# Optimization experiments

Measured on AMD Instinct MI355X. Metric: run time of the kernel, lower is better.

Reference implementation:

```python
import jax, jax.numpy as jnp
import numpy as np

NTYPE = 4
NWAVE = 8
NORBIT = 128
NIPSIN = 3
CUTOFF = 5.0
NEIGH = 64
NB = 32
NATOM = 256
NPAIR_PER = NATOM * NEIGH  # pairs per molecule

# index_para: [0, 1,1,1, 2,...x9] -> length 1 + 3 + 9 = 13
INDEX_PARA = np.concatenate([np.zeros(1, np.int32)] + [np.full(3 ** i, i, np.int32) for i in range(1, NIPSIN)])
NPARA = INDEX_PARA.shape[0]  # 13


def setup_inputs() -> dict:
    key = jax.random.key(0)
    ks = jax.random.split(key, 12)
    cart = jax.random.normal(ks[0], (NB, NATOM, 3), dtype=jnp.float32)
    numatoms = jnp.full((NB,), NATOM, dtype=jnp.int32)
    species = jax.random.randint(ks[1], (NB * NATOM,), 0, NTYPE, dtype=jnp.int32)
    atom_index = jax.random.randint(ks[2], (2, NB, NPAIR_PER), 0, NATOM, dtype=jnp.int32)
    # small nonzero shifts so no pair has exactly zero distance
    shifts = 0.1 * jax.random.normal(ks[3], (NB, NPAIR_PER, 3), dtype=jnp.float32)
    rs = jax.random.uniform(ks[4], (NTYPE, NWAVE), dtype=jnp.float32) * CUTOFF
    inta = -jnp.abs(jax.random.normal(ks[5], (NTYPE, NWAVE), dtype=jnp.float32))
    params = jnp.ones((NTYPE, NWAVE), dtype=jnp.float32) / float(NEIGH)
    hyper = 0.1 * jax.random.normal(ks[6], (NIPSIN, NWAVE, NORBIT), dtype=jnp.float32)
    oc_w0 = 0.05 * jax.random.normal(ks[7], (NORBIT, NWAVE), dtype=jnp.float32)
    oc_e0 = 0.05 * jax.random.normal(ks[8], (NTYPE, NWAVE), dtype=jnp.float32)
    oc_w1 = 0.05 * jax.random.normal(ks[9], (NORBIT, NWAVE), dtype=jnp.float32)
    oc_e1 = 0.05 * jax.random.normal(ks[10], (NTYPE, NWAVE), dtype=jnp.float32)
    return {"cart": cart, "shifts": shifts, "rs": rs, "inta": inta, "params": params,
            "hyper": hyper, "oc_w0": oc_w0, "oc_e0": oc_e0, "oc_w1": oc_w1, "oc_e1": oc_e1,
            "numatoms": numatoms, "species": species, "atom_index": atom_index}


def _angular(dist_vec, f_cut):
    # dist_vec: (N, 3), f_cut: (N,) -> (NPARA, N)
    dv = dist_vec.T  # (3, N)
    ang = f_cut[None, :]  # (1, N)
    parts = [ang]
    for _ in range(1, NIPSIN):
        ang = (ang[:, None, :] * dv[None, :, :]).reshape(-1, ang.shape[-1])
        parts.append(ang)
    return jnp.concatenate(parts, axis=0)  # (13, N)


def reference(cart, shifts, rs, inta, params, hyper, oc_w0, oc_e0, oc_w1, oc_e1,
              numatoms, species, atom_index):
    nbatch, numatom, _ = cart.shape
    totnatom = nbatch * numatom
    # global pair indices: per-molecule neighbor indices + molecule offset
    offsets = jnp.arange(nbatch, dtype=atom_index.dtype) * numatom  # (nbatch,)
    idx12 = (atom_index + offsets[None, :, None]).reshape(2, -1)  # (2, Npair)
    cart_ = cart.reshape(-1, 3)  # (totnatom, 3)
    dist_vec = cart_[idx12[0]] - cart_[idx12[1]] + shifts.reshape(-1, 3)  # (Npair, 3)
    distances = jnp.linalg.norm(dist_vec, axis=-1)  # (Npair,)
    f_cut = jnp.square(0.5 * jnp.cos(distances * (jnp.pi / CUTOFF)) + 0.5)
    sp_pair = species[idx12[1]]  # (Npair,)
    # radial gaussian: exp(inta * (d - rs)^2), per-pair type gather
    radial = jnp.exp(inta[sp_pair] * jnp.square(distances[:, None] - rs[sp_pair]))  # (Npair, nwave)
    ang = _angular(dist_vec, f_cut)  # (NPARA, Npair)
    # orbital[i, j, k] = ang[j, i] * radial[i, k]
    orbital = ang.T[:, :, None] * radial[:, None, :]  # (Npair, NPARA, nwave)
    hyper_exp = hyper[jnp.asarray(INDEX_PARA)]  # (NPARA, nwave, norbit)

    def obtain(orb_coeff):
        worbital = orbital * orb_coeff[idx12[1]][:, None, :]  # gather + scale
        sum_worbital = jax.ops.segment_sum(worbital, idx12[0], num_segments=totnatom)
        hyper_worbital = jnp.einsum('ijk,jkm->ijm', sum_worbital, hyper_exp)
        return jnp.sum(jnp.square(hyper_worbital), axis=1)  # (totnatom, norbit)

    orb_coeff = params[species]  # (totnatom, nwave)
    density = obtain(orb_coeff)
    for w, e in ((oc_w0, oc_e0), (oc_w1, oc_e1)):
        orb_coeff = orb_coeff + jnp.tanh(density @ w + e[species])
        density = obtain(orb_coeff)
    return density
```

## Files before the change

### kernel.cpp

```cpp
#include <hip/hip_runtime.h>
#include <hip/hip_bf16.h>
#include <math.h>

#define NTYPE   4
#define NWAVE   8
#define NORBIT  128
#define NEIGH   64
#define NB      32
#define NATOM   256
#define NPP     (NATOM * NEIGH)
#define NPAIR   (NB * NPP)
#define TOTATOM (NB * NATOM)
#define NPARA   13

#define CHUNK   2048
#define BPB     8
#define NBLK    (NB * BPB)

__device__ __forceinline__ float fast_tanh(float x) {
    float ax = fabsf(x);
    float e  = __expf(-2.0f * ax);
    float r  = (1.0f - e) / (1.0f + e);
    return copysignf(r, x);
}

__global__ __launch_bounds__(256) void k_hist(const int* __restrict__ atom_index,
                                              int* __restrict__ histpart) {
    const int bl = blockIdx.x, t = threadIdx.x;
    const int b = bl >> 3, c = bl & 7;
    __shared__ int hist[NATOM];
    hist[t] = 0;
    __syncthreads();
    const int base = b * NPP + c * CHUNK;
#pragma unroll
    for (int k = 0; k < CHUNK / 256; k++) {
        int i = atom_index[base + t + k * 256];
        atomicAdd(&hist[i], 1);
    }
    __syncthreads();
    histpart[bl * NATOM + t] = hist[t];
}

__global__ __launch_bounds__(256) void k_offsets(const int* __restrict__ histpart,
                                                 int* __restrict__ startpart,
                                                 int* __restrict__ offs,
                                                 const int* __restrict__ species,
                                                 const float* __restrict__ params,
                                                 float* __restrict__ coeff0) {
    const int b = blockIdx.x, t = threadIdx.x;
    int h[BPB];
    int tot = 0;
#pragma unroll
    for (int c = 0; c < BPB; c++) {
        h[c] = histpart[(b * BPB + c) * NATOM + t];
        tot += h[c];
    }
    __shared__ int scan[NATOM];
    scan[t] = tot;
    __syncthreads();
    for (int d = 1; d < NATOM; d <<= 1) {
        int v = (t >= d) ? scan[t - d] : 0;
        __syncthreads();
        scan[t] += v;
        __syncthreads();
    }
    int run = b * NPP + (scan[t] - tot);
    offs[b * NATOM + t] = run;
    if (b == 0 && t == 0) offs[TOTATOM] = NPAIR;
#pragma unroll
    for (int c = 0; c < BPB; c++) {
        startpart[(b * BPB + c) * NATOM + t] = run;
        run += h[c];
    }
    int a = b * NATOM + t;
    int sp = species[a];
#pragma unroll
    for (int w = 0; w < NWAVE; w++) coeff0[a * NWAVE + w] = params[sp * NWAVE + w];
}

__global__ __launch_bounds__(256) void k_scatter(const int* __restrict__ atom_index,
                                                 const float* __restrict__ cart,
                                                 const float* __restrict__ shifts,
                                                 const int* __restrict__ species,
                                                 const int* __restrict__ startpart,
                                                 float4* __restrict__ rec) {
    const int bl = blockIdx.x, t = threadIdx.x;
    const int b = bl >> 3, c = bl & 7;
    __shared__ int cur[NATOM];
    __shared__ float cx[NATOM], cy[NATOM], cz[NATOM];
    __shared__ int spl[NATOM];
    cur[t] = startpart[bl * NATOM + t];
    const int ag = b * NATOM + t;
    cx[t] = cart[ag * 3 + 0];
    cy[t] = cart[ag * 3 + 1];
    cz[t] = cart[ag * 3 + 2];
    spl[t] = species[ag];
    __syncthreads();
    const int base = b * NPP + c * CHUNK;
#pragma unroll
    for (int k = 0; k < CHUNK / 256; k++) {
        int p = base + t + k * 256;
        int i = atom_index[p];
        int j = atom_index[NPAIR + p];
        float dx = cx[i] - cx[j] + shifts[p * 3 + 0];
        float dy = cy[i] - cy[j] + shifts[p * 3 + 1];
        float dz = cz[i] - cz[j] + shifts[p * 3 + 2];
        int jg = b * NATOM + j;
        int pos = atomicAdd(&cur[i], 1);
        rec[pos] = make_float4(dx, dy, dz, __int_as_float(jg | (spl[j] << 16)));
    }
}

__global__ __launch_bounds__(256) void k_density(const float4* __restrict__ rec,
                                                 const int* __restrict__ offs,
                                                 const float* __restrict__ coeff_in,
                                                 const float* __restrict__ rs,
                                                 const float* __restrict__ inta,
                                                 const float* __restrict__ hyper,
                                                 const float* __restrict__ W,
                                                 const float* __restrict__ E,
                                                 const int* __restrict__ species,
                                                 float* __restrict__ coeff_out,
                                                 float* __restrict__ density_out,
                                                 int mode) {
    const int wv = threadIdx.x >> 6;
    const int lane = threadIdx.x & 63;
    const int a = blockIdx.x * 4 + wv;
    const int pl = lane >> 3;
    const int w  = lane & 7;

    float rs0 = rs[w],      rs1 = rs[8 + w],  rs2 = rs[16 + w], rs3 = rs[24 + w];
    float in0 = inta[w],    in1 = inta[8 + w], in2 = inta[16 + w], in3 = inta[24 + w];

    const int start = offs[a];
    const int end   = offs[a + 1];

    float S[NPARA];
#pragma unroll
    for (int k = 0; k < NPARA; k++) S[k] = 0.0f;

    int idx = start + pl;
    float4 r = make_float4(0.f, 0.f, 0.f, 0.f);
    if (idx < end) r = rec[idx];
    for (; idx < end; idx += 8) {
        int nidx = idx + 8;
        float4 rn = r;
        if (nidx < end) rn = rec[nidx];
        int jp = __float_as_int(r.w);
        int j  = jp & 0xFFFF;
        int sp = jp >> 16;
        float cj = coeff_in[j * NWAVE + w];
        float d2 = r.x * r.x + r.y * r.y + r.z * r.z;
        float d  = sqrtf(d2);
        float c  = __cosf(d * 0.62831853071795864769f);
        float fc = 0.5f * c + 0.5f;
        fc = fc * fc;
        float rw = (sp == 0) ? rs0 : (sp == 1) ? rs1 : (sp == 2) ? rs2 : rs3;
        float iw = (sp == 0) ? in0 : (sp == 1) ? in1 : (sp == 2) ? in2 : in3;
        float dr  = d - rw;
        float rad = __expf(iw * dr * dr);
        float q = fc * rad * cj;
        S[0] += q;
        float qx = q * r.x, qy = q * r.y, qz = q * r.z;
        S[1] += qx; S[2] += qy; S[3] += qz;
        S[4]  += qx * r.x; S[5]  += qx * r.y; S[6]  += qx * r.z;
        S[7]  += qy * r.x; S[8]  += qy * r.y; S[9]  += qy * r.z;
        S[10] += qz * r.x; S[11] += qz * r.y; S[12] += qz * r.z;
        r = rn;
    }

#pragma unroll
    for (int k = 0; k < NPARA; k++) {
        S[k] += __shfl_xor(S[k], 8, 64);
        S[k] += __shfl_xor(S[k], 16, 64);
        S[k] += __shfl_xor(S[k], 32, 64);
    }

    __shared__ float lds_S[4][NWAVE * 16];
    if (pl == 0) {
#pragma unroll
        for (int k = 0; k < NPARA; k++) lds_S[wv][w * 16 + k] = S[k];
    }
    __syncthreads();

    const int o0 = lane, o1 = lane + 64;
    float hw0[NPARA], hw1[NPARA];
#pragma unroll
    for (int k = 0; k < NPARA; k++) { hw0[k] = 0.0f; hw1[k] = 0.0f; }
#pragma unroll
    for (int w2 = 0; w2 < NWAVE; w2++) {
        const float* Sw = &lds_S[wv][w2 * 16];
        float4 s0 = *(const float4*)(Sw);
        float4 s1 = *(const float4*)(Sw + 4);
        float4 s2 = *(const float4*)(Sw + 8);
        float  sc = Sw[12];
        float h00 = hyper[w2 * NORBIT + o0];
        float h01 = hyper[w2 * NORBIT + o1];
        float h10 = hyper[(NWAVE + w2) * NORBIT + o0];
        float h11 = hyper[(NWAVE + w2) * NORBIT + o1];
        float h20 = hyper[(2 * NWAVE + w2) * NORBIT + o0];
        float h21 = hyper[(2 * NWAVE + w2) * NORBIT + o1];
        hw0[0]  += s0.x * h00; hw1[0]  += s0.x * h01;
        hw0[1]  += s0.y * h10; hw1[1]  += s0.y * h11;
        hw0[2]  += s0.z * h10; hw1[2]  += s0.z * h11;
        hw0[3]  += s0.w * h10; hw1[3]  += s0.w * h11;
        hw0[4]  += s1.x * h20; hw1[4]  += s1.x * h21;
        hw0[5]  += s1.y * h20; hw1[5]  += s1.y * h21;
        hw0[6]  += s1.z * h20; hw1[6]  += s1.z * h21;
        hw0[7]  += s1.w * h20; hw1[7]  += s1.w * h21;
        hw0[8]  += s2.x * h20; hw1[8]  += s2.x * h21;
        hw0[9]  += s2.y * h20; hw1[9]  += s2.y * h21;
        hw0[10] += s2.z * h20; hw1[10] += s2.z * h21;
        hw0[11] += s2.w * h20; hw1[11] += s2.w * h21;
        hw0[12] += sc   * h20; hw1[12] += sc   * h21;
    }
    float acc0 = 0.0f, acc1 = 0.0f;
#pragma unroll
    for (int k = 0; k < NPARA; k++) {
        acc0 += hw0[k] * hw0[k];
        acc1 += hw1[k] * hw1[k];
    }

    if (mode == 1) {
        density_out[a * NORBIT + o0] = acc0;
        density_out[a * NORBIT + o1] = acc1;
        return;
    }

    float part[NWAVE];
#pragma unroll
    for (int w2 = 0; w2 < NWAVE; w2++)
        part[w2] = acc0 * W[o0 * NWAVE + w2] + acc1 * W[o1 * NWAVE + w2];
#pragma unroll
    for (int mask = 1; mask < 64; mask <<= 1) {
#pragma unroll
        for (int w2 = 0; w2 < NWAVE; w2++)
            part[w2] += __shfl_xor(part[w2], mask, 64);
    }
    if (lane < NWAVE) {
        int sp = species[a];
        coeff_out[a * NWAVE + lane] =
            coeff_in[a * NWAVE + lane] + fast_tanh(part[lane] + E[sp * NWAVE + lane]);
    }
}

extern "C" void kernel_launch(void* const* d_in, const int* in_sizes, int n_in,
                              void* d_out, int out_size, void* d_ws, size_t ws_size,
                              hipStream_t stream) {
    const float* cart    = (const float*)d_in[0];
    const float* shifts  = (const float*)d_in[1];
    const float* rs      = (const float*)d_in[2];
    const float* inta    = (const float*)d_in[3];
    const float* params  = (const float*)d_in[4];
    const float* hyper   = (const float*)d_in[5];
    const float* w0      = (const float*)d_in[6];
    const float* e0      = (const float*)d_in[7];
    const float* w1      = (const float*)d_in[8];
    const float* e1      = (const float*)d_in[9];
    const int* species    = (const int*)d_in[11];
    const int* atom_index = (const int*)d_in[12];
    float* out = (float*)d_out;

    char* ws = (char*)d_ws;
    float4* rec    = (float4*)ws;  ws += (size_t)NPAIR * 16;
    float* coeffA  = (float*)ws;   ws += (size_t)TOTATOM * NWAVE * 4;
    float* coeffB  = (float*)ws;   ws += (size_t)TOTATOM * NWAVE * 4;
    int* offs      = (int*)ws;     ws += (TOTATOM + 1) * 4;
    ws = (char*)(((uintptr_t)ws + 255) & ~(uintptr_t)255);
    int* histpart  = (int*)ws;     ws += (size_t)NBLK * NATOM * 4;
    int* startpart = (int*)ws;     ws += (size_t)NBLK * NATOM * 4;

    k_hist<<<NBLK, 256, 0, stream>>>(atom_index, histpart);
    k_offsets<<<NB, 256, 0, stream>>>(histpart, startpart, offs, species, params, coeffA);
    k_scatter<<<NBLK, 256, 0, stream>>>(atom_index, cart, shifts, species, startpart, rec);

    k_density<<<TOTATOM / 4, 256, 0, stream>>>(rec, offs, coeffA, rs, inta, hyper,
                                               w0, e0, species, coeffB, out, 0);
    k_density<<<TOTATOM / 4, 256, 0, stream>>>(rec, offs, coeffB, rs, inta, hyper,
                                               w1, e1, species, coeffA, out, 0);
    k_density<<<TOTATOM / 4, 256, 0, stream>>>(rec, offs, coeffA, rs, inta, hyper,
                                               w1, e1, species, coeffB, out, 1);
}
```

Measured before the change: 150.0 us.

## Fuse all pipeline stages into one cooperative persistent kernel with grid syncs

Replaces the six separate launches (histogram, offsets, scatter, three density rounds) with one cooperative kernel of 1024 blocks that separates the stages with grid.sync. Each block handles a 512-pair chunk and 8 atoms per density round, so launch gaps and inter-kernel drains are removed. The original multi-kernel path stays as a fallback if the cooperative launch fails. The grid syncs and fences add their own cost. The smaller grid for the density rounds (1024 blocks instead of 2048) may reduce latency hiding.

```diff
diff --git a/kernel.cpp b/kernel.cpp
--- a/kernel.cpp
+++ b/kernel.cpp
@@ -1,6 +1,8 @@
 #include <hip/hip_runtime.h>
-#include <hip/hip_bf16.h>
+#include <hip/hip_cooperative_groups.h>
 #include <math.h>
+
+namespace cg = cooperative_groups;
 
 #define NTYPE   4
 #define NWAVE   8
@@ -13,9 +15,14 @@
 #define TOTATOM (NB * NATOM)
 #define NPARA   13
 
-#define CHUNK   2048
-#define BPB     8
+#define CHUNK   512
+#define BPB     32
 #define NBLK    (NB * BPB)
+#define APB     (TOTATOM / NBLK)
+
+#define FB_CHUNK  2048
+#define FB_BPB    8
+#define FB_NBLK   (NB * FB_BPB)
 
 __device__ __forceinline__ float fast_tanh(float x) {
     float ax = fabsf(x);
@@ -23,6 +30,234 @@
     float r  = (1.0f - e) / (1.0f + e);
     return copysignf(r, x);
 }
+
+__global__ __launch_bounds__(256, 4) void k_fused(
+    const int* __restrict__ atom_index, const float* __restrict__ cart,
+    const float* __restrict__ shifts, const int* __restrict__ species,
+    const float* __restrict__ rs, const float* __restrict__ inta,
+    const float* __restrict__ params, const float* __restrict__ hyper,
+    const float* __restrict__ W0, const float* __restrict__ E0,
+    const float* __restrict__ W1, const float* __restrict__ E1,
+    float* __restrict__ density_out, float4* __restrict__ rec,
+    float* __restrict__ coeffA, float* __restrict__ coeffB,
+    int* __restrict__ offs, int* __restrict__ histpart,
+    int* __restrict__ startpart)
+{
+    cg::grid_group grid = cg::this_grid();
+    const int bl = blockIdx.x, t = threadIdx.x;
+    const int b = bl >> 5, c = bl & 31;
+    const int base = b * NPP + c * CHUNK;
+
+    __shared__ int   ibuf[NATOM];
+    __shared__ int   cur[NATOM];
+    __shared__ float cx[NATOM], cy[NATOM], cz[NATOM];
+    __shared__ int   spl[NATOM];
+    __shared__ float lds_S[4][NWAVE * 16];
+
+    ibuf[t] = 0;
+    __syncthreads();
+#pragma unroll
+    for (int k = 0; k < CHUNK / 256; k++)
+        atomicAdd(&ibuf[atom_index[base + t + k * 256]], 1);
+    __syncthreads();
+    histpart[bl * NATOM + t] = ibuf[t];
+    __threadfence();
+    grid.sync();
+    __threadfence();
+
+    if (bl < NB) {
+        int h[BPB];
+        int tot = 0;
+#pragma unroll
+        for (int c2 = 0; c2 < BPB; c2++) {
+            h[c2] = histpart[(bl * BPB + c2) * NATOM + t];
+            tot += h[c2];
+        }
+        ibuf[t] = tot;
+        __syncthreads();
+        for (int d = 1; d < NATOM; d <<= 1) {
+            int v = (t >= d) ? ibuf[t - d] : 0;
+            __syncthreads();
+            ibuf[t] += v;
+            __syncthreads();
+        }
+        int run = bl * NPP + ibuf[t] - tot;
+        offs[bl * NATOM + t] = run;
+        if (bl == 0 && t == 0) offs[TOTATOM] = NPAIR;
+#pragma unroll
+        for (int c2 = 0; c2 < BPB; c2++) {
+            startpart[(bl * BPB + c2) * NATOM + t] = run;
+            run += h[c2];
+        }
+        int a = bl * NATOM + t;
+        int sp = species[a];
+#pragma unroll
+        for (int w = 0; w < NWAVE; w++)
+            coeffA[a * NWAVE + w] = params[sp * NWAVE + w];
+    }
+    __threadfence();
+    grid.sync();
+    __threadfence();
+
+    cur[t] = startpart[bl * NATOM + t];
+    const int ag = b * NATOM + t;
+    cx[t] = cart[ag * 3 + 0];
+    cy[t] = cart[ag * 3 + 1];
+    cz[t] = cart[ag * 3 + 2];
+    spl[t] = species[ag];
+    __syncthreads();
+#pragma unroll
+    for (int k = 0; k < CHUNK / 256; k++) {
+        int p = base + t + k * 256;
+        int i = atom_index[p];
+        int j = atom_index[NPAIR + p];
+        float dx = cx[i] - cx[j] + shifts[p * 3 + 0];
+        float dy = cy[i] - cy[j] + shifts[p * 3 + 1];
+        float dz = cz[i] - cz[j] + shifts[p * 3 + 2];
+        int jg = b * NATOM + j;
+        int pos = atomicAdd(&cur[i], 1);
+        rec[pos] = make_float4(dx, dy, dz, __int_as_float(jg | (spl[j] << 16)));
+    }
+    __threadfence();
+    grid.sync();
+    __threadfence();
+
+    const int wv = t >> 6;
+    const int lane = t & 63;
+    const int pl = lane >> 3;
+    const int w  = lane & 7;
+    const int o0 = lane, o1 = lane + 64;
+
+    const float rs0 = rs[w],      rs1 = rs[8 + w],  rs2 = rs[16 + w], rs3 = rs[24 + w];
+    const float in0 = inta[w],    in1 = inta[8 + w], in2 = inta[16 + w], in3 = inta[24 + w];
+
+    for (int round = 0; round < 3; round++) {
+        const float* cin  = (round == 1) ? coeffB : coeffA;
+        float*       cout = (round == 0) ? coeffB : coeffA;
+        const float* Wm   = (round == 0) ? W0 : W1;
+        const float* Em   = (round == 0) ? E0 : E1;
+        const int    mode = (round == 2) ? 1 : 0;
+
+#pragma unroll
+        for (int g = 0; g < APB / 4; g++) {
+            const int a = bl * APB + g * 4 + wv;
+            const int start = offs[a];
+            const int end   = offs[a + 1];
+
+            float S[NPARA];
+#pragma unroll
+            for (int k = 0; k < NPARA; k++) S[k] = 0.0f;
+
+            int idx = start + pl;
+            float4 r = make_float4(0.f, 0.f, 0.f, 0.f);
+            if (idx < end) r = rec[idx];
+            for (; idx < end; idx += 8) {
+                int nidx = idx + 8;
+                float4 rn = r;
+                if (nidx < end) rn = rec[nidx];
+                int jp = __float_as_int(r.w);
+                int j  = jp & 0xFFFF;
+                int sp = jp >> 16;
+                float cj = cin[j * NWAVE + w];
+                float d2 = r.x * r.x + r.y * r.y + r.z * r.z;
+                float d  = sqrtf(d2);
+                float cc = __cosf(d * 0.62831853071795864769f);
+                float fc = 0.5f * cc + 0.5f;
+                fc = fc * fc;
+                float rw = (sp == 0) ? rs0 : (sp == 1) ? rs1 : (sp == 2) ? rs2 : rs3;
+                float iw = (sp == 0) ? in0 : (sp == 1) ? in1 : (sp == 2) ? in2 : in3;
+                float dr  = d - rw;
+                float rad = __expf(iw * dr * dr);
+                float q = fc * rad * cj;
+                S[0] += q;
+                float qx = q * r.x, qy = q * r.y, qz = q * r.z;
+                S[1] += qx; S[2] += qy; S[3] += qz;
+                S[4]  += qx * r.x; S[5]  += qx * r.y; S[6]  += qx * r.z;
+                S[7]  += qy * r.x; S[8]  += qy * r.y; S[9]  += qy * r.z;
+                S[10] += qz * r.x; S[11] += qz * r.y; S[12] += qz * r.z;
+                r = rn;
+            }
+
+#pragma unroll
+            for (int k = 0; k < NPARA; k++) {
+                S[k] += __shfl_xor(S[k], 8, 64);
+                S[k] += __shfl_xor(S[k], 16, 64);
+                S[k] += __shfl_xor(S[k], 32, 64);
+            }
+
+            if (pl == 0) {
+#pragma unroll
+                for (int k = 0; k < NPARA; k++) lds_S[wv][w * 16 + k] = S[k];
+            }
+            __syncthreads();
+
+            float hw0[NPARA], hw1[NPARA];
+#pragma unroll
+            for (int k = 0; k < NPARA; k++) { hw0[k] = 0.0f; hw1[k] = 0.0f; }
+#pragma unroll
+            for (int w2 = 0; w2 < NWAVE; w2++) {
+                const float* Sw = &lds_S[wv][w2 * 16];
+                float4 s0 = *(const float4*)(Sw);
+                float4 s1 = *(const float4*)(Sw + 4);
+                float4 s2 = *(const float4*)(Sw + 8);
+                float  sc = Sw[12];
+                float h00 = hyper[w2 * NORBIT + o0];
+                float h01 = hyper[w2 * NORBIT + o1];
+                float h10 = hyper[(NWAVE + w2) * NORBIT + o0];
+                float h11 = hyper[(NWAVE + w2) * NORBIT + o1];
+                float h20 = hyper[(2 * NWAVE + w2) * NORBIT + o0];
+                float h21 = hyper[(2 * NWAVE + w2) * NORBIT + o1];
+                hw0[0]  += s0.x * h00; hw1[0]  += s0.x * h01;
+                hw0[1]  += s0.y * h10; hw1[1]  += s0.y * h11;
+                hw0[2]  += s0.z * h10; hw1[2]  += s0.z * h11;
+                hw0[3]  += s0.w * h10; hw1[3]  += s0.w * h11;
+                hw0[4]  += s1.x * h20; hw1[4]  += s1.x * h21;
+                hw0[5]  += s1.y * h20; hw1[5]  += s1.y * h21;
+                hw0[6]  += s1.z * h20; hw1[6]  += s1.z * h21;
+                hw0[7]  += s1.w * h20; hw1[7]  += s1.w * h21;
+                hw0[8]  += s2.x * h20; hw1[8]  += s2.x * h21;
+                hw0[9]  += s2.y * h20; hw1[9]  += s2.y * h21;
+                hw0[10] += s2.z * h20; hw1[10] += s2.z * h21;
+                hw0[11] += s2.w * h20; hw1[11] += s2.w * h21;
+                hw0[12] += sc   * h20; hw1[12] += sc   * h21;
+            }
+            float acc0 = 0.0f, acc1 = 0.0f;
+#pragma unroll
+            for (int k = 0; k < NPARA; k++) {
+                acc0 += hw0[k] * hw0[k];
+                acc1 += hw1[k] * hw1[k];
+            }
+
+            if (mode == 1) {
+                density_out[a * NORBIT + o0] = acc0;
+                density_out[a * NORBIT + o1] = acc1;
+            } else {
+                float part[NWAVE];
+#pragma unroll
+                for (int w2 = 0; w2 < NWAVE; w2++)
+                    part[w2] = acc0 * Wm[o0 * NWAVE + w2] + acc1 * Wm[o1 * NWAVE + w2];
+#pragma unroll
+                for (int mask = 1; mask < 64; mask <<= 1) {
+#pragma unroll
+                    for (int w2 = 0; w2 < NWAVE; w2++)
+                        part[w2] += __shfl_xor(part[w2], mask, 64);
+                }
+                if (lane < NWAVE) {
+                    int sp = species[a];
+                    cout[a * NWAVE + lane] =
+                        cin[a * NWAVE + lane] + fast_tanh(part[lane] + Em[sp * NWAVE + lane]);
+                }
+            }
+            __syncthreads();
+        }
+        if (round < 2) {
+            __threadfence();
+            grid.sync();
+            __threadfence();
+        }
+    }
+}
+
 
 __global__ __launch_bounds__(256) void k_hist(const int* __restrict__ atom_index,
                                               int* __restrict__ histpart) {
@@ -31,9 +266,9 @@
     __shared__ int hist[NATOM];
     hist[t] = 0;
     __syncthreads();
-    const int base = b * NPP + c * CHUNK;
-#pragma unroll
-    for (int k = 0; k < CHUNK / 256; k++) {
+    const int base = b * NPP + c * FB_CHUNK;
+#pragma unroll
+    for (int k = 0; k < FB_CHUNK / 256; k++) {
         int i = atom_index[base + t + k * 256];
         atomicAdd(&hist[i], 1);
     }
@@ -48,11 +283,11 @@
                                                  const float* __restrict__ params,
                                                  float* __restrict__ coeff0) {
     const int b = blockIdx.x, t = threadIdx.x;
-    int h[BPB];
+    int h[FB_BPB];
     int tot = 0;
 #pragma unroll
-    for (int c = 0; c < BPB; c++) {
-        h[c] = histpart[(b * BPB + c) * NATOM + t];
+    for (int c = 0; c < FB_BPB; c++) {
+        h[c] = histpart[(b * FB_BPB + c) * NATOM + t];
         tot += h[c];
     }
     __shared__ int scan[NATOM];
@@ -68,8 +303,8 @@
     offs[b * NATOM + t] = run;
     if (b == 0 && t == 0) offs[TOTATOM] = NPAIR;
 #pragma unroll
-    for (int c = 0; c < BPB; c++) {
-        startpart[(b * BPB + c) * NATOM + t] = run;
+    for (int c = 0; c < FB_BPB; c++) {
+        startpart[(b * FB_BPB + c) * NATOM + t] = run;
         run += h[c];
     }
     int a = b * NATOM + t;
@@ -96,9 +331,9 @@
     cz[t] = cart[ag * 3 + 2];
     spl[t] = species[ag];
     __syncthreads();
-    const int base = b * NPP + c * CHUNK;
-#pragma unroll
-    for (int k = 0; k < CHUNK / 256; k++) {
+    const int base = b * NPP + c * FB_CHUNK;
+#pragma unroll
+    for (int k = 0; k < FB_CHUNK / 256; k++) {
         int p = base + t + k * 256;
         int i = atom_index[p];
         int j = atom_index[NPAIR + p];
@@ -270,9 +505,25 @@
     int* histpart  = (int*)ws;     ws += (size_t)NBLK * NATOM * 4;
     int* startpart = (int*)ws;     ws += (size_t)NBLK * NATOM * 4;
 
-    k_hist<<<NBLK, 256, 0, stream>>>(atom_index, histpart);
+    static int coop_ok = -1;
+    if (coop_ok != 0) {
+        void* args[] = {
+            (void*)&atom_index, (void*)&cart, (void*)&shifts, (void*)&species,
+            (void*)&rs, (void*)&inta, (void*)&params, (void*)&hyper,
+            (void*)&w0, (void*)&e0, (void*)&w1, (void*)&e1,
+            (void*)&out, (void*)&rec, (void*)&coeffA, (void*)&coeffB,
+            (void*)&offs, (void*)&histpart, (void*)&startpart
+        };
+        hipError_t err = hipLaunchCooperativeKernel((const void*)k_fused,
+                                                    dim3(NBLK), dim3(256),
+                                                    args, 0, stream);
+        if (err == hipSuccess) { coop_ok = 1; return; }
+        coop_ok = 0;
+    }
+
+    k_hist<<<FB_NBLK, 256, 0, stream>>>(atom_index, histpart);
     k_offsets<<<NB, 256, 0, stream>>>(histpart, startpart, offs, species, params, coeffA);
-    k_scatter<<<NBLK, 256, 0, stream>>>(atom_index, cart, shifts, species, startpart, rec);
+    k_scatter<<<FB_NBLK, 256, 0, stream>>>(atom_index, cart, shifts, species, startpart, rec);
 
     k_density<<<TOTATOM / 4, 256, 0, stream>>>(rec, offs, coeffA, rs, inta, hyper,
                                                w0, e0, species, coeffB, out, 0);
```

Result: no change. 149.8 us (-0.1%).
